# Kernel optimization log

Hardware: AMD Instinct MI355X
Metric: run time of the kernel (lower is better)

Reference implementation:

```python
import jax, jax.numpy as jnp
import numpy as np

EPS = 1e-5

def _layernorm(x, g, b):
    m = jnp.mean(x, axis=-1, keepdims=True)
    v = jnp.mean(jnp.square(x - m), axis=-1, keepdims=True)
    return (x - m) * jax.lax.rsqrt(v + EPS) * g + b

def setup_inputs() -> dict:
    key = jax.random.key(0)
    ks = jax.random.split(key, 8)
    B, T, C, H, D = 4096, 16, 512, 8, 64
    s = 0.02
    return {
        "x": jax.random.normal(ks[0], (B, T, C), jnp.float32),
        "ln1_g": jnp.ones((C,), jnp.float32),
        "ln1_b": jnp.zeros((C,), jnp.float32),
        "wq": jax.random.normal(ks[1], (H, C, D), jnp.float32) * s,
        "wk": jax.random.normal(ks[2], (H, C, D), jnp.float32) * s,
        "wv": jax.random.normal(ks[3], (H, C, D), jnp.float32) * s,
        "w_proj": jax.random.normal(ks[4], (H * D, C), jnp.float32) * s,
        "b_proj": jnp.zeros((C,), jnp.float32),
        "ln2_g": jnp.ones((C,), jnp.float32),
        "ln2_b": jnp.zeros((C,), jnp.float32),
        "w1": jax.random.normal(ks[5], (C, 4 * C), jnp.float32) * s,
        "b1": jnp.zeros((4 * C,), jnp.float32),
        "w2": jax.random.normal(ks[6], (4 * C, C), jnp.float32) * s,
        "b2": jnp.zeros((C,), jnp.float32),
    }

def reference(x, ln1_g, ln1_b, wq, wk, wv, w_proj, b_proj, ln2_g, ln2_b, w1, b1, w2, b2):
    B, T, C = x.shape
    H, _, D = wq.shape
    h = _layernorm(x, ln1_g, ln1_b)
    # fused per-head projections (original looped over 8 Head modules)
    q = jnp.einsum('btc,hcd->bhtd', h, wq)
    k = jnp.einsum('btc,hcd->bhtd', h, wk)
    v = jnp.einsum('btc,hcd->bhtd', h, wv)
    logits = jnp.einsum('bhtd,bhsd->bhts', q, k) * (D ** -0.5)
    causal = jnp.tril(jnp.ones((T, T), bool))
    logits = jnp.where(causal, logits, -jnp.inf)
    att = jax.nn.softmax(logits, axis=-1)  # dropout is identity at eval
    o = jnp.einsum('bhts,bhsd->bhtd', att, v)
    o = o.transpose(0, 2, 1, 3).reshape(B, T, H * D)  # concat heads in order
    y = o @ w_proj + b_proj + x  # residual 1
    h2 = _layernorm(y, ln2_g, ln2_b)
    f = jax.nn.relu(h2 @ w1 + b1) @ w2 + b2
    return f + y  # residual 2
```

## Files before the change

kernel.cpp:

```cpp
#include <hip/hip_runtime.h>
#include <hip/hip_bf16.h>

typedef __attribute__((ext_vector_type(8))) short s16x8;
typedef __attribute__((ext_vector_type(4))) float f32x4;

#define GAS __attribute__((address_space(1)))
#define LAS __attribute__((address_space(3)))

__device__ __forceinline__ float b2f(unsigned short u) {
  union { unsigned int i; float f; } x; x.i = ((unsigned int)u) << 16; return x.f;
}
__device__ __forceinline__ unsigned short f2b(float f) {
  union { float f; unsigned int i; } x; x.f = f;
  unsigned int r = x.i + 0x7fffu + ((x.i >> 16) & 1u);
  return (unsigned short)(r >> 16);
}

__device__ __forceinline__ void gl16(const unsigned short* g, unsigned short* l) {
  __builtin_amdgcn_global_load_lds((const GAS unsigned int*)g,
                                   (LAS unsigned int*)l, 16, 0, 0);
}

__global__ __launch_bounds__(256) void pack_qkv_k(const float* __restrict__ wq,
                                                  const float* __restrict__ wk,
                                                  const float* __restrict__ wv,
                                                  unsigned short* __restrict__ dst) {
  int idx = blockIdx.x * 256 + threadIdx.x;
  int n = idx >> 9, c = idx & 511;
  int sel = n >> 9;
  int hn = n & 511;
  const float* src = sel == 0 ? wq : (sel == 1 ? wk : wv);
  float v = src[((hn >> 6) << 15) + (c << 6) + (hn & 63)];
  dst[idx] = f2b(v);
}

__global__ __launch_bounds__(256) void pack_T_k(const float* __restrict__ src,
                                                unsigned short* __restrict__ dst,
                                                int K, int N) {
  int idx = blockIdx.x * 256 + threadIdx.x;
  int n = idx / K, k = idx % K;
  dst[idx] = f2b(src[(long long)k * N + n]);
}

__global__ __launch_bounds__(256) void ln_k(const float* __restrict__ in,
                                            const float* __restrict__ g,
                                            const float* __restrict__ bb,
                                            unsigned short* __restrict__ out) {
  int row = blockIdx.x * 4 + (threadIdx.x >> 6);
  int lane = threadIdx.x & 63;
  const float* p = in + (size_t)row * 512 + lane * 8;
  f32x4 a = *(const f32x4*)p;
  f32x4 b = *(const f32x4*)(p + 4);
  float vals[8] = {a.x, a.y, a.z, a.w, b.x, b.y, b.z, b.w};
  float s = 0.f, q = 0.f;
#pragma unroll
  for (int i = 0; i < 8; i++) { s += vals[i]; q += vals[i] * vals[i]; }
#pragma unroll
  for (int off = 1; off < 64; off <<= 1) {
    s += __shfl_xor(s, off);
    q += __shfl_xor(q, off);
  }
  float mean = s * (1.0f / 512.0f);
  float rstd = rsqrtf(q * (1.0f / 512.0f) - mean * mean + 1e-5f);
  const float* gp = g + lane * 8;
  const float* bp = bb + lane * 8;
  s16x8 o;
#pragma unroll
  for (int i = 0; i < 8; i++) o[i] = (short)f2b((vals[i] - mean) * rstd * gp[i] + bp[i]);
  *(s16x8*)(out + (size_t)row * 512 + lane * 8) = o;
}

__global__ __launch_bounds__(256) void ln_b_k(const unsigned short* __restrict__ in,
                                              const float* __restrict__ g,
                                              const float* __restrict__ bb,
                                              unsigned short* __restrict__ out) {
  int row = blockIdx.x * 4 + (threadIdx.x >> 6);
  int lane = threadIdx.x & 63;
  s16x8 v8 = *(const s16x8*)(in + (size_t)row * 512 + lane * 8);
  float vals[8];
#pragma unroll
  for (int i = 0; i < 8; i++) vals[i] = b2f((unsigned short)v8[i]);
  float s = 0.f, q = 0.f;
#pragma unroll
  for (int i = 0; i < 8; i++) { s += vals[i]; q += vals[i] * vals[i]; }
#pragma unroll
  for (int off = 1; off < 64; off <<= 1) {
    s += __shfl_xor(s, off);
    q += __shfl_xor(q, off);
  }
  float mean = s * (1.0f / 512.0f);
  float rstd = rsqrtf(q * (1.0f / 512.0f) - mean * mean + 1e-5f);
  const float* gp = g + lane * 8;
  const float* bp = bb + lane * 8;
  s16x8 o;
#pragma unroll
  for (int i = 0; i < 8; i++) o[i] = (short)f2b((vals[i] - mean) * rstd * gp[i] + bp[i]);
  *(s16x8*)(out + (size_t)row * 512 + lane * 8) = o;
}

__global__ __launch_bounds__(256) void attn_k(const unsigned short* __restrict__ qkv,
                                              unsigned short* __restrict__ o) {
  int w = (blockIdx.x << 2) + (threadIdx.x >> 6);
  int lane = threadIdx.x & 63;
  int b = w >> 3, h = w & 7;
  int t = lane >> 2, p = lane & 3;

  size_t rowq = (size_t)(b * 16 + t) * 1536 + h * 64 + p * 16;
  float q[16];
  {
    s16x8 q0 = *(const s16x8*)(qkv + rowq);
    s16x8 q1 = *(const s16x8*)(qkv + rowq + 8);
#pragma unroll
    for (int i = 0; i < 8; i++) {
      q[i] = b2f((unsigned short)q0[i]) * 0.125f;
      q[8 + i] = b2f((unsigned short)q1[i]) * 0.125f;
    }
  }
  float lg[16];
  size_t kbase = (size_t)(b * 16) * 1536 + 512 + h * 64 + p * 16;
#pragma unroll
  for (int s = 0; s < 16; s++) {
    const unsigned short* kp = qkv + kbase + (size_t)s * 1536;
    s16x8 k0 = *(const s16x8*)kp;
    s16x8 k1 = *(const s16x8*)(kp + 8);
    float d = 0.f;
#pragma unroll
    for (int i = 0; i < 8; i++)
      d += q[i] * b2f((unsigned short)k0[i]) + q[8 + i] * b2f((unsigned short)k1[i]);
    d += __shfl_xor(d, 1);
    d += __shfl_xor(d, 2);
    lg[s] = d;
  }
  float mx = -1e30f;
#pragma unroll
  for (int s = 0; s < 16; s++)
    if (s <= t) mx = fmaxf(mx, lg[s]);
  float den = 0.f;
#pragma unroll
  for (int s = 0; s < 16; s++) {
    float e = (s <= t) ? __expf(lg[s] - mx) : 0.f;
    lg[s] = e;
    den += e;
  }
  float inv = 1.f / den;
  float acc[16] = {};
  size_t vbase = kbase + 512;
#pragma unroll
  for (int s = 0; s < 16; s++) {
    const unsigned short* vp = qkv + vbase + (size_t)s * 1536;
    s16x8 v0 = *(const s16x8*)vp;
    s16x8 v1 = *(const s16x8*)(vp + 8);
    float a = lg[s] * inv;
#pragma unroll
    for (int i = 0; i < 8; i++) {
      acc[i] += a * b2f((unsigned short)v0[i]);
      acc[8 + i] += a * b2f((unsigned short)v1[i]);
    }
  }
  size_t orow = (size_t)(b * 16 + t) * 512 + h * 64 + p * 16;
  s16x8 r0, r1;
#pragma unroll
  for (int i = 0; i < 8; i++) {
    r0[i] = (short)f2b(acc[i]);
    r1[i] = (short)f2b(acc[8 + i]);
  }
  *(s16x8*)(o + orow) = r0;
  *(s16x8*)(o + orow + 8) = r1;
}

enum { EPI_BF16 = 0, EPI_RESF32 = 1, EPI_RELU_BF16 = 2, EPI_YB = 3, EPI_OUTB = 4 };

template <int EPI>
__global__ __launch_bounds__(256) void gemm_bt(
    const unsigned short* __restrict__ A,
    const unsigned short* __restrict__ Bt,
    int K, int N, int nT,
    const float* __restrict__ bias, const void* __restrict__ res,
    float* __restrict__ outF, unsigned short* __restrict__ outB) {
  __shared__ __align__(16) unsigned short As[2][128 * 32];
  __shared__ __align__(16) unsigned short Bs[2][128 * 32];

  int tid = threadIdx.x;
  int lid = ((int)blockIdx.x & 7) * ((int)gridDim.x >> 3) + ((int)blockIdx.x >> 3);
  int mBase = (lid / nT) * 128;
  int nBase = (lid % nT) * 128;

  int lane = tid & 63;
  int wv = tid >> 6;
  int wr = (wv >> 1) * 64, wc = (wv & 1) * 64;
  int l15 = lane & 15;
  int lr4 = (lane >> 4) * 4;
  int fc = (((lane >> 4) ^ ((l15 >> 1) & 3)) << 3);

  int sr = tid >> 2;
  int gc = (((tid & 3) ^ ((tid >> 3) & 3)) << 3);
  const unsigned short* pa = A + (size_t)(mBase + sr) * K + gc;
  const unsigned short* pb = Bt + (size_t)(nBase + sr) * K + gc;
  size_t rowskip = (size_t)64 * K;

  f32x4 acc[4][4] = {};

  auto stage = [&](int b, int kt) {
    unsigned short* lA = &As[b][wv * 512];
    unsigned short* lB = &Bs[b][wv * 512];
    gl16(pa + kt, lA);
    gl16(pa + kt + rowskip, lA + 2048);
    gl16(pb + kt, lB);
    gl16(pb + kt + rowskip, lB + 2048);
  };

  stage(0, 0);
  __syncthreads();
  int cur = 0;
  for (int kt = 0; kt < K; kt += 32) {
    if (kt + 32 < K) stage(cur ^ 1, kt + 32);
    s16x8 af[4], bf[4];
#pragma unroll
    for (int m = 0; m < 4; m++)
      af[m] = *(const s16x8*)&As[cur][(wr + m * 16 + l15) * 32 + fc];
#pragma unroll
    for (int n = 0; n < 4; n++)
      bf[n] = *(const s16x8*)&Bs[cur][(wc + n * 16 + l15) * 32 + fc];
#pragma unroll
    for (int m = 0; m < 4; m++)
#pragma unroll
      for (int n = 0; n < 4; n++)
        acc[m][n] = __builtin_amdgcn_mfma_f32_16x16x32_bf16(af[m], bf[n], acc[m][n], 0, 0, 0);
    __syncthreads();
    cur ^= 1;
  }

#pragma unroll
  for (int n = 0; n < 4; n++) {
    int gc2 = nBase + wc + n * 16 + l15;
    float bv = (EPI == EPI_BF16) ? 0.f : bias[gc2];
#pragma unroll
    for (int m = 0; m < 4; m++) {
#pragma unroll
      for (int j = 0; j < 4; j++) {
        int gr = mBase + wr + m * 16 + lr4 + j;
        size_t off = (size_t)gr * N + gc2;
        float v = acc[m][n][j] + bv;
        if (EPI == EPI_RESF32)
          outF[off] = v + ((const float*)res)[off];
        else if (EPI == EPI_YB)
          outB[off] = f2b(v + ((const float*)res)[off]);
        else if (EPI == EPI_OUTB)
          outF[off] = v + b2f(((const unsigned short*)res)[off]);
        else if (EPI == EPI_RELU_BF16)
          outB[off] = f2b(fmaxf(v, 0.f));
        else
          outB[off] = f2b(v);
      }
    }
  }
}

extern "C" void kernel_launch(void* const* d_in, const int* in_sizes, int n_in,
                              void* d_out, int out_size, void* d_ws, size_t ws_size,
                              hipStream_t stream) {
  const float* x      = (const float*)d_in[0];
  const float* ln1_g  = (const float*)d_in[1];
  const float* ln1_b  = (const float*)d_in[2];
  const float* wq     = (const float*)d_in[3];
  const float* wk     = (const float*)d_in[4];
  const float* wv     = (const float*)d_in[5];
  const float* w_proj = (const float*)d_in[6];
  const float* b_proj = (const float*)d_in[7];
  const float* ln2_g  = (const float*)d_in[8];
  const float* ln2_b  = (const float*)d_in[9];
  const float* w1     = (const float*)d_in[10];
  const float* b1     = (const float*)d_in[11];
  const float* w2     = (const float*)d_in[12];
  const float* b2     = (const float*)d_in[13];
  float* out = (float*)d_out;

  char* ws = (char*)d_ws;
  unsigned short* qkvT  = (unsigned short*)(ws + 0);
  unsigned short* projT = (unsigned short*)(ws + 1572864);
  unsigned short* w1T   = (unsigned short*)(ws + 2097152);
  unsigned short* w2T   = (unsigned short*)(ws + 4194304);
  unsigned short* hbuf  = (unsigned short*)(ws + 6291456);
  unsigned short* qkv   = (unsigned short*)(ws + 73400320);
  unsigned short* obuf  = (unsigned short*)(ws + 341835776);
  unsigned short* ybuf  = (unsigned short*)(ws + 408944640);
  bool yb16 = ws_size >= 476053504ull;

  pack_qkv_k<<<3072, 256, 0, stream>>>(wq, wk, wv, qkvT);
  pack_T_k<<<1024, 256, 0, stream>>>(w_proj, projT, 512, 512);
  pack_T_k<<<4096, 256, 0, stream>>>(w1, w1T, 512, 2048);
  pack_T_k<<<4096, 256, 0, stream>>>(w2, w2T, 2048, 512);

  ln_k<<<16384, 256, 0, stream>>>(x, ln1_g, ln1_b, hbuf);

  gemm_bt<EPI_BF16><<<6144, 256, 0, stream>>>(hbuf, qkvT, 512, 1536, 12,
                                              nullptr, nullptr, nullptr, qkv);
  attn_k<<<8192, 256, 0, stream>>>(qkv, obuf);

  unsigned short* ff = qkv;
  if (yb16) {
    gemm_bt<EPI_YB><<<2048, 256, 0, stream>>>(obuf, projT, 512, 512, 4,
                                              b_proj, x, nullptr, ybuf);
    ln_b_k<<<16384, 256, 0, stream>>>(ybuf, ln2_g, ln2_b, hbuf);
    gemm_bt<EPI_RELU_BF16><<<8192, 256, 0, stream>>>(hbuf, w1T, 512, 2048, 16,
                                                     b1, nullptr, nullptr, ff);
    gemm_bt<EPI_OUTB><<<2048, 256, 0, stream>>>(ff, w2T, 2048, 512, 4,
                                                b2, ybuf, out, nullptr);
  } else {
    gemm_bt<EPI_RESF32><<<2048, 256, 0, stream>>>(obuf, projT, 512, 512, 4,
                                                  b_proj, x, out, nullptr);
    ln_k<<<16384, 256, 0, stream>>>(out, ln2_g, ln2_b, hbuf);
    gemm_bt<EPI_RELU_BF16><<<8192, 256, 0, stream>>>(hbuf, w1T, 512, 2048, 16,
                                                     b1, nullptr, nullptr, ff);
    gemm_bt<EPI_RESF32><<<2048, 256, 0, stream>>>(ff, w2T, 2048, 512, 4,
                                                  b2, out, out, nullptr);
  }
}
```

Before: 891.3 us.

## Enlarge GEMM tiles to 256x256 with 512 threads and BK=64

Rewrites the bf16 GEMM to use 256x256 output tiles per block with 8 waves, each computing 128x64, and a K-step of 64 with an XOR-swizzled LDS layout. It replaces the plain __syncthreads with an explicit vmcnt wait plus barriers so the next tile's global-to-LDS loads overlap compute. The goal is more operand reuse per load and fewer global and LDS loads per MFMA. In exchange it uses 128 KB of LDS and more accumulator registers per thread, and it launches far fewer blocks, which lowers occupancy and may leave CUs idle on the smaller GEMMs.

Result: slower. 980.2 us (+10.0%).

```diff
diff --git a/kernel.cpp b/kernel.cpp
--- a/kernel.cpp
+++ b/kernel.cpp
@@ -6,6 +6,9 @@
 
 #define GAS __attribute__((address_space(1)))
 #define LAS __attribute__((address_space(3)))
+
+#define WAITV(N) asm volatile("s_waitcnt vmcnt(" #N ")" ::: "memory")
+#define BAR() __builtin_amdgcn_s_barrier()
 
 __device__ __forceinline__ float b2f(unsigned short u) {
   union { unsigned int i; float f; } x; x.i = ((unsigned int)u) << 16; return x.f;
@@ -171,74 +174,104 @@
 enum { EPI_BF16 = 0, EPI_RESF32 = 1, EPI_RELU_BF16 = 2, EPI_YB = 3, EPI_OUTB = 4 };
 
 template <int EPI>
-__global__ __launch_bounds__(256) void gemm_bt(
+__global__ __launch_bounds__(512, 2) void gemm_bt(
     const unsigned short* __restrict__ A,
     const unsigned short* __restrict__ Bt,
     int K, int N, int nT,
     const float* __restrict__ bias, const void* __restrict__ res,
     float* __restrict__ outF, unsigned short* __restrict__ outB) {
-  __shared__ __align__(16) unsigned short As[2][128 * 32];
-  __shared__ __align__(16) unsigned short Bs[2][128 * 32];
+  __shared__ __align__(16) unsigned short As[2][2][128 * 64];
+  __shared__ __align__(16) unsigned short Bs[2][2][128 * 64];
 
   int tid = threadIdx.x;
   int lid = ((int)blockIdx.x & 7) * ((int)gridDim.x >> 3) + ((int)blockIdx.x >> 3);
-  int mBase = (lid / nT) * 128;
-  int nBase = (lid % nT) * 128;
+  int mBase = (lid / nT) * 256;
+  int nBase = (lid % nT) * 256;
 
   int lane = tid & 63;
-  int wv = tid >> 6;
-  int wr = (wv >> 1) * 64, wc = (wv & 1) * 64;
+  int wid = tid >> 6;
+  int wm = wid >> 2;
+  int wn = wid & 3;
   int l15 = lane & 15;
-  int lr4 = (lane >> 4) * 4;
-  int fc = (((lane >> 4) ^ ((l15 >> 1) & 3)) << 3);
-
-  int sr = tid >> 2;
-  int gc = (((tid & 3) ^ ((tid >> 3) & 3)) << 3);
-  const unsigned short* pa = A + (size_t)(mBase + sr) * K + gc;
-  const unsigned short* pb = Bt + (size_t)(nBase + sr) * K + gc;
-  size_t rowskip = (size_t)64 * K;
-
-  f32x4 acc[4][4] = {};
-
-  auto stage = [&](int b, int kt) {
-    unsigned short* lA = &As[b][wv * 512];
-    unsigned short* lB = &Bs[b][wv * 512];
-    gl16(pa + kt, lA);
-    gl16(pa + kt + rowskip, lA + 2048);
-    gl16(pb + kt, lB);
-    gl16(pb + kt + rowskip, lB + 2048);
+  int s4 = lane >> 4;
+  int lr4 = s4 * 4;
+
+  int srow = tid >> 3;
+  int scol = ((tid & 7) ^ (srow & 7)) << 3;
+  const unsigned short* pa = A + (size_t)(mBase + srow) * K + scol;
+  const unsigned short* pb = Bt + (size_t)(nBase + srow) * K + scol;
+  unsigned short* sbA = &As[0][0][0] + wid * 512;
+  unsigned short* sbB = &Bs[0][0][0] + wid * 512;
+  size_t k64 = (size_t)64 * K;
+
+  f32x4 acc[8][4] = {};
+
+  auto stage = [&](int buf, int kt) {
+    unsigned short* dA = sbA + buf * 16384;
+    unsigned short* dB = sbB + buf * 16384;
+    gl16(pa + kt, dA);
+    gl16(pa + kt + k64, dA + 4096);
+    gl16(pa + kt + 2 * k64, dA + 8192);
+    gl16(pa + kt + 3 * k64, dA + 12288);
+    gl16(pb + kt, dB);
+    gl16(pb + kt + k64, dB + 4096);
+    gl16(pb + kt + 2 * k64, dB + 8192);
+    gl16(pb + kt + 3 * k64, dB + 12288);
   };
 
+  auto compute = [&](int buf) {
+    const unsigned short* hA = &As[buf][wm][0];
+    const unsigned short* hB = &Bs[buf][wn >> 1][0];
+    int rb0 = (wn & 1) * 64;
+#pragma unroll
+    for (int kk = 0; kk < 2; ++kk) {
+      int xs = (((kk * 4 + s4) ^ (l15 & 7)) << 3);
+      s16x8 bfr[4], afr[4];
+#pragma unroll
+      for (int n = 0; n < 4; ++n)
+        bfr[n] = *(const s16x8*)&hB[(rb0 + n * 16 + l15) * 64 + xs];
+#pragma unroll
+      for (int m = 0; m < 4; ++m)
+        afr[m] = *(const s16x8*)&hA[(m * 16 + l15) * 64 + xs];
+#pragma unroll
+      for (int m = 0; m < 4; ++m)
+#pragma unroll
+        for (int n = 0; n < 4; ++n)
+          acc[m][n] = __builtin_amdgcn_mfma_f32_16x16x32_bf16(afr[m], bfr[n], acc[m][n], 0, 0, 0);
+#pragma unroll
+      for (int m = 0; m < 4; ++m)
+        afr[m] = *(const s16x8*)&hA[((m + 4) * 16 + l15) * 64 + xs];
+#pragma unroll
+      for (int m = 0; m < 4; ++m)
+#pragma unroll
+        for (int n = 0; n < 4; ++n)
+          acc[m + 4][n] = __builtin_amdgcn_mfma_f32_16x16x32_bf16(afr[m], bfr[n], acc[m + 4][n], 0, 0, 0);
+    }
+  };
+
+  int NT = K >> 6;
   stage(0, 0);
-  __syncthreads();
-  int cur = 0;
-  for (int kt = 0; kt < K; kt += 32) {
-    if (kt + 32 < K) stage(cur ^ 1, kt + 32);
-    s16x8 af[4], bf[4];
-#pragma unroll
-    for (int m = 0; m < 4; m++)
-      af[m] = *(const s16x8*)&As[cur][(wr + m * 16 + l15) * 32 + fc];
-#pragma unroll
-    for (int n = 0; n < 4; n++)
-      bf[n] = *(const s16x8*)&Bs[cur][(wc + n * 16 + l15) * 32 + fc];
-#pragma unroll
-    for (int m = 0; m < 4; m++)
-#pragma unroll
-      for (int n = 0; n < 4; n++)
-        acc[m][n] = __builtin_amdgcn_mfma_f32_16x16x32_bf16(af[m], bf[n], acc[m][n], 0, 0, 0);
-    __syncthreads();
-    cur ^= 1;
+  for (int t = 0; t < NT; ++t) {
+    if (t + 1 < NT) {
+      stage((t + 1) & 1, (t + 1) << 6);
+      WAITV(8);
+    } else {
+      WAITV(0);
+    }
+    BAR();
+    compute(t & 1);
+    BAR();
   }
 
 #pragma unroll
   for (int n = 0; n < 4; n++) {
-    int gc2 = nBase + wc + n * 16 + l15;
+    int gc2 = nBase + wn * 64 + n * 16 + l15;
     float bv = (EPI == EPI_BF16) ? 0.f : bias[gc2];
 #pragma unroll
-    for (int m = 0; m < 4; m++) {
+    for (int m = 0; m < 8; m++) {
 #pragma unroll
       for (int j = 0; j < 4; j++) {
-        int gr = mBase + wr + m * 16 + lr4 + j;
+        int gr = mBase + wm * 128 + m * 16 + lr4 + j;
         size_t off = (size_t)gr * N + gc2;
         float v = acc[m][n][j] + bv;
         if (EPI == EPI_RESF32)
@@ -293,26 +326,26 @@
 
   ln_k<<<16384, 256, 0, stream>>>(x, ln1_g, ln1_b, hbuf);
 
-  gemm_bt<EPI_BF16><<<6144, 256, 0, stream>>>(hbuf, qkvT, 512, 1536, 12,
+  gemm_bt<EPI_BF16><<<1536, 512, 0, stream>>>(hbuf, qkvT, 512, 1536, 6,
                                               nullptr, nullptr, nullptr, qkv);
   attn_k<<<8192, 256, 0, stream>>>(qkv, obuf);
 
   unsigned short* ff = qkv;
   if (yb16) {
-    gemm_bt<EPI_YB><<<2048, 256, 0, stream>>>(obuf, projT, 512, 512, 4,
-                                              b_proj, x, nullptr, ybuf);
+    gemm_bt<EPI_YB><<<512, 512, 0, stream>>>(obuf, projT, 512, 512, 2,
+                                             b_proj, x, nullptr, ybuf);
     ln_b_k<<<16384, 256, 0, stream>>>(ybuf, ln2_g, ln2_b, hbuf);
-    gemm_bt<EPI_RELU_BF16><<<8192, 256, 0, stream>>>(hbuf, w1T, 512, 2048, 16,
+    gemm_bt<EPI_RELU_BF16><<<2048, 512, 0, stream>>>(hbuf, w1T, 512, 2048, 8,
                                                      b1, nullptr, nullptr, ff);
-    gemm_bt<EPI_OUTB><<<2048, 256, 0, stream>>>(ff, w2T, 2048, 512, 4,
-                                                b2, ybuf, out, nullptr);
+    gemm_bt<EPI_OUTB><<<512, 512, 0, stream>>>(ff, w2T, 2048, 512, 2,
+                                               b2, ybuf, out, nullptr);
   } else {
-    gemm_bt<EPI_RESF32><<<2048, 256, 0, stream>>>(obuf, projT, 512, 512, 4,
-                                                  b_proj, x, out, nullptr);
+    gemm_bt<EPI_RESF32><<<512, 512, 0, stream>>>(obuf, projT, 512, 512, 2,
+                                                 b_proj, x, out, nullptr);
     ln_k<<<16384, 256, 0, stream>>>(out, ln2_g, ln2_b, hbuf);
-    gemm_bt<EPI_RELU_BF16><<<8192, 256, 0, stream>>>(hbuf, w1T, 512, 2048, 16,
+    gemm_bt<EPI_RELU_BF16><<<2048, 512, 0, stream>>>(hbuf, w1T, 512, 2048, 8,
                                                      b1, nullptr, nullptr, ff);
-    gemm_bt<EPI_RESF32><<<2048, 256, 0, stream>>>(ff, w2T, 2048, 512, 4,
-                                                  b2, out, out, nullptr);
-  }
-}
+    gemm_bt<EPI_RESF32><<<512, 512, 0, stream>>>(ff, w2T, 2048, 512, 2,
+                                                 b2, out, out, nullptr);
+  }
+}
```

## Stage GEMM epilogue through LDS for vectorized bf16 stores, single-buffer K loop

Applied to the files above, without the earlier changes.

The GEMM drops double-buffered LDS staging in favour of a single buffer with two barriers per K step. This shrinks shared memory, which may raise occupancy, but the global loads no longer overlap with the MFMA work. The bf16-output epilogues now transpose accumulators through LDS so each lane writes 4 contiguous bf16 values instead of scattered 2-byte stores. Input x is converted once to bf16 and reused for LN1 and as the bf16 residual in the projection epilogue, which cuts fp32 reads but adds rounding of the residual.

Measured after the change: 914.0 us. 1.03x slower.

```diff
diff --git a/kernel.cpp b/kernel.cpp
--- a/kernel.cpp
+++ b/kernel.cpp
@@ -2,10 +2,13 @@
 #include <hip/hip_bf16.h>
 
 typedef __attribute__((ext_vector_type(8))) short s16x8;
+typedef __attribute__((ext_vector_type(4))) short s16x4;
 typedef __attribute__((ext_vector_type(4))) float f32x4;
 
 #define GAS __attribute__((address_space(1)))
 #define LAS __attribute__((address_space(3)))
+
+#define WAITL() asm volatile("s_waitcnt lgkmcnt(0)" ::: "memory")
 
 __device__ __forceinline__ float b2f(unsigned short u) {
   union { unsigned int i; float f; } x; x.i = ((unsigned int)u) << 16; return x.f;
@@ -19,6 +22,18 @@
 __device__ __forceinline__ void gl16(const unsigned short* g, unsigned short* l) {
   __builtin_amdgcn_global_load_lds((const GAS unsigned int*)g,
                                    (LAS unsigned int*)l, 16, 0, 0);
+}
+
+__global__ __launch_bounds__(256) void pack_x_k(const float* __restrict__ x,
+                                                unsigned short* __restrict__ xb) {
+  size_t i = ((size_t)blockIdx.x * 256 + threadIdx.x) * 8;
+  f32x4 a = *(const f32x4*)(x + i);
+  f32x4 b = *(const f32x4*)(x + i + 4);
+  float vals[8] = {a.x, a.y, a.z, a.w, b.x, b.y, b.z, b.w};
+  s16x8 o;
+#pragma unroll
+  for (int k = 0; k < 8; k++) o[k] = (short)f2b(vals[k]);
+  *(s16x8*)(xb + i) = o;
 }
 
 __global__ __launch_bounds__(256) void pack_qkv_k(const float* __restrict__ wq,
@@ -168,7 +183,7 @@
   *(s16x8*)(o + orow + 8) = r1;
 }
 
-enum { EPI_BF16 = 0, EPI_RESF32 = 1, EPI_RELU_BF16 = 2, EPI_YB = 3, EPI_OUTB = 4 };
+enum { EPI_BF16 = 0, EPI_RESF32 = 1, EPI_RELU = 2, EPI_YBB = 3, EPI_OUTB = 4 };
 
 template <int EPI>
 __global__ __launch_bounds__(256) void gemm_bt(
@@ -177,8 +192,9 @@
     int K, int N, int nT,
     const float* __restrict__ bias, const void* __restrict__ res,
     float* __restrict__ outF, unsigned short* __restrict__ outB) {
-  __shared__ __align__(16) unsigned short As[2][128 * 32];
-  __shared__ __align__(16) unsigned short Bs[2][128 * 32];
+  __shared__ __align__(16) unsigned char SM[17408];
+  unsigned short* As = (unsigned short*)SM;
+  unsigned short* Bs = (unsigned short*)(SM + 8192);
 
   int tid = threadIdx.x;
   int lid = ((int)blockIdx.x & 7) * ((int)gridDim.x >> 3) + ((int)blockIdx.x >> 3);
@@ -189,69 +205,93 @@
   int wv = tid >> 6;
   int wr = (wv >> 1) * 64, wc = (wv & 1) * 64;
   int l15 = lane & 15;
-  int lr4 = (lane >> 4) * 4;
-  int fc = (((lane >> 4) ^ ((l15 >> 1) & 3)) << 3);
+  int s4 = lane >> 4;
+  int lr4 = s4 * 4;
+  int fc = ((s4 ^ ((l15 >> 1) & 3)) << 3);
 
   int sr = tid >> 2;
   int gc = (((tid & 3) ^ ((tid >> 3) & 3)) << 3);
   const unsigned short* pa = A + (size_t)(mBase + sr) * K + gc;
   const unsigned short* pb = Bt + (size_t)(nBase + sr) * K + gc;
+  unsigned short* lA = As + wv * 512;
+  unsigned short* lB = Bs + wv * 512;
   size_t rowskip = (size_t)64 * K;
 
   f32x4 acc[4][4] = {};
 
-  auto stage = [&](int b, int kt) {
-    unsigned short* lA = &As[b][wv * 512];
-    unsigned short* lB = &Bs[b][wv * 512];
+  for (int kt = 0; kt < K; kt += 32) {
+    __syncthreads();
     gl16(pa + kt, lA);
     gl16(pa + kt + rowskip, lA + 2048);
     gl16(pb + kt, lB);
     gl16(pb + kt + rowskip, lB + 2048);
-  };
-
-  stage(0, 0);
-  __syncthreads();
-  int cur = 0;
-  for (int kt = 0; kt < K; kt += 32) {
-    if (kt + 32 < K) stage(cur ^ 1, kt + 32);
+    __syncthreads();
     s16x8 af[4], bf[4];
 #pragma unroll
-    for (int m = 0; m < 4; m++)
-      af[m] = *(const s16x8*)&As[cur][(wr + m * 16 + l15) * 32 + fc];
-#pragma unroll
-    for (int n = 0; n < 4; n++)
-      bf[n] = *(const s16x8*)&Bs[cur][(wc + n * 16 + l15) * 32 + fc];
+    for (int m = 0; m < 4; m++) af[m] = *(const s16x8*)&As[(wr + m * 16 + l15) * 32 + fc];
+#pragma unroll
+    for (int n = 0; n < 4; n++) bf[n] = *(const s16x8*)&Bs[(wc + n * 16 + l15) * 32 + fc];
 #pragma unroll
     for (int m = 0; m < 4; m++)
 #pragma unroll
       for (int n = 0; n < 4; n++)
         acc[m][n] = __builtin_amdgcn_mfma_f32_16x16x32_bf16(af[m], bf[n], acc[m][n], 0, 0, 0);
-    __syncthreads();
-    cur ^= 1;
-  }
-
-#pragma unroll
-  for (int n = 0; n < 4; n++) {
-    int gc2 = nBase + wc + n * 16 + l15;
-    float bv = (EPI == EPI_BF16) ? 0.f : bias[gc2];
+  }
+  __syncthreads();
+
+  if (EPI == EPI_RESF32 || EPI == EPI_OUTB) {
+#pragma unroll
+    for (int n = 0; n < 4; n++) {
+      int gc2 = nBase + wc + n * 16 + l15;
+      float bv = bias[gc2];
+#pragma unroll
+      for (int m = 0; m < 4; m++) {
+#pragma unroll
+        for (int j = 0; j < 4; j++) {
+          int gr = mBase + wr + m * 16 + lr4 + j;
+          size_t off = (size_t)gr * N + gc2;
+          float v = acc[m][n][j] + bv;
+          if (EPI == EPI_RESF32)
+            outF[off] = v + ((const float*)res)[off];
+          else
+            outF[off] = v + b2f(((const unsigned short*)res)[off]);
+        }
+      }
+    }
+  } else {
+    float* ep = (float*)SM + wv * 1088;
+    int colc = nBase + wc + l15 * 4;
+    f32x4 bias4 = {0.f, 0.f, 0.f, 0.f};
+    if (EPI != EPI_BF16) bias4 = *(const f32x4*)&bias[colc];
 #pragma unroll
     for (int m = 0; m < 4; m++) {
 #pragma unroll
-      for (int j = 0; j < 4; j++) {
-        int gr = mBase + wr + m * 16 + lr4 + j;
-        size_t off = (size_t)gr * N + gc2;
-        float v = acc[m][n][j] + bv;
-        if (EPI == EPI_RESF32)
-          outF[off] = v + ((const float*)res)[off];
-        else if (EPI == EPI_YB)
-          outB[off] = f2b(v + ((const float*)res)[off]);
-        else if (EPI == EPI_OUTB)
-          outF[off] = v + b2f(((const unsigned short*)res)[off]);
-        else if (EPI == EPI_RELU_BF16)
-          outB[off] = f2b(fmaxf(v, 0.f));
-        else
-          outB[off] = f2b(v);
+      for (int n = 0; n < 4; n++)
+#pragma unroll
+        for (int j = 0; j < 4; j++)
+          ep[(lr4 + j) * 68 + n * 16 + l15] = acc[m][n][j];
+      WAITL();
+#pragma unroll
+      for (int rd = 0; rd < 4; rd++) {
+        int r = s4 + 4 * rd;
+        f32x4 v = *(const f32x4*)&ep[r * 68 + l15 * 4];
+        v.x += bias4.x; v.y += bias4.y; v.z += bias4.z; v.w += bias4.w;
+        int gr = mBase + wr + m * 16 + r;
+        size_t off = (size_t)gr * N + colc;
+        if (EPI == EPI_YBB) {
+          s16x4 rb = *(const s16x4*)((const unsigned short*)res + off);
+          v.x += b2f((unsigned short)rb[0]); v.y += b2f((unsigned short)rb[1]);
+          v.z += b2f((unsigned short)rb[2]); v.w += b2f((unsigned short)rb[3]);
+        } else if (EPI == EPI_RELU) {
+          v.x = fmaxf(v.x, 0.f); v.y = fmaxf(v.y, 0.f);
+          v.z = fmaxf(v.z, 0.f); v.w = fmaxf(v.w, 0.f);
+        }
+        s16x4 o;
+        o[0] = (short)f2b(v.x); o[1] = (short)f2b(v.y);
+        o[2] = (short)f2b(v.z); o[3] = (short)f2b(v.w);
+        *(s16x4*)(outB + off) = o;
       }
+      WAITL();
     }
   }
 }
@@ -282,6 +322,7 @@
   unsigned short* w2T   = (unsigned short*)(ws + 4194304);
   unsigned short* hbuf  = (unsigned short*)(ws + 6291456);
   unsigned short* qkv   = (unsigned short*)(ws + 73400320);
+  unsigned short* xb    = (unsigned short*)(ws + 274726912);
   unsigned short* obuf  = (unsigned short*)(ws + 341835776);
   unsigned short* ybuf  = (unsigned short*)(ws + 408944640);
   bool yb16 = ws_size >= 476053504ull;
@@ -291,27 +332,30 @@
   pack_T_k<<<4096, 256, 0, stream>>>(w1, w1T, 512, 2048);
   pack_T_k<<<4096, 256, 0, stream>>>(w2, w2T, 2048, 512);
 
-  ln_k<<<16384, 256, 0, stream>>>(x, ln1_g, ln1_b, hbuf);
-
-  gemm_bt<EPI_BF16><<<6144, 256, 0, stream>>>(hbuf, qkvT, 512, 1536, 12,
-                                              nullptr, nullptr, nullptr, qkv);
-  attn_k<<<8192, 256, 0, stream>>>(qkv, obuf);
-
   unsigned short* ff = qkv;
   if (yb16) {
-    gemm_bt<EPI_YB><<<2048, 256, 0, stream>>>(obuf, projT, 512, 512, 4,
-                                              b_proj, x, nullptr, ybuf);
+    pack_x_k<<<16384, 256, 0, stream>>>(x, xb);
+    ln_b_k<<<16384, 256, 0, stream>>>(xb, ln1_g, ln1_b, hbuf);
+    gemm_bt<EPI_BF16><<<6144, 256, 0, stream>>>(hbuf, qkvT, 512, 1536, 12,
+                                                nullptr, nullptr, nullptr, qkv);
+    attn_k<<<8192, 256, 0, stream>>>(qkv, obuf);
+    gemm_bt<EPI_YBB><<<2048, 256, 0, stream>>>(obuf, projT, 512, 512, 4,
+                                               b_proj, xb, nullptr, ybuf);
     ln_b_k<<<16384, 256, 0, stream>>>(ybuf, ln2_g, ln2_b, hbuf);
-    gemm_bt<EPI_RELU_BF16><<<8192, 256, 0, stream>>>(hbuf, w1T, 512, 2048, 16,
-                                                     b1, nullptr, nullptr, ff);
+    gemm_bt<EPI_RELU><<<8192, 256, 0, stream>>>(hbuf, w1T, 512, 2048, 16,
+                                                b1, nullptr, nullptr, ff);
     gemm_bt<EPI_OUTB><<<2048, 256, 0, stream>>>(ff, w2T, 2048, 512, 4,
                                                 b2, ybuf, out, nullptr);
   } else {
+    ln_k<<<16384, 256, 0, stream>>>(x, ln1_g, ln1_b, hbuf);
+    gemm_bt<EPI_BF16><<<6144, 256, 0, stream>>>(hbuf, qkvT, 512, 1536, 12,
+                                                nullptr, nullptr, nullptr, qkv);
+    attn_k<<<8192, 256, 0, stream>>>(qkv, obuf);
     gemm_bt<EPI_RESF32><<<2048, 256, 0, stream>>>(obuf, projT, 512, 512, 4,
                                                   b_proj, x, out, nullptr);
     ln_k<<<16384, 256, 0, stream>>>(out, ln2_g, ln2_b, hbuf);
-    gemm_bt<EPI_RELU_BF16><<<8192, 256, 0, stream>>>(hbuf, w1T, 512, 2048, 16,
-                                                     b1, nullptr, nullptr, ff);
+    gemm_bt<EPI_RELU><<<8192, 256, 0, stream>>>(hbuf, w1T, 512, 2048, 16,
+                                                b1, nullptr, nullptr, ff);
     gemm_bt<EPI_RESF32><<<2048, 256, 0, stream>>>(ff, w2T, 2048, 512, 4,
                                                   b2, out, out, nullptr);
   }
```
